# Kernel optimization log

Measured on AMD Instinct MI355X. Metric: run time of the kernel, lower is better.

## Reference

```python
import jax, jax.numpy as jnp
import numpy as np

B, P, K, F, H = 128, 200, 60, 4, 64   # events, points/event, knn k, feat dim, hidden
N = B * P


def setup_inputs() -> dict:
    key = jax.random.key(0)
    k0, k1, k2, k3 = jax.random.split(key, 4)
    x = jax.random.normal(k0, (N, F), jnp.float32)
    pos = jax.random.normal(k1, (N, 3), jnp.float32)
    batch = jnp.arange(N, dtype=jnp.int32) // P  # sorted event ids, equal-size events
    W1 = jax.random.normal(k2, (F + 3, H), jnp.float32) / np.sqrt(F + 3)
    b1 = jnp.zeros((H,), jnp.float32)
    W2 = jax.random.normal(k3, (H, H), jnp.float32) / np.sqrt(H)
    b2 = jnp.zeros((H,), jnp.float32)
    return {"x": x, "pos": pos, "batch": batch, "W1": W1, "b1": b1, "W2": W2, "b2": b2}


def _knn_edges(pos):
    """knn_graph(pos, K, batch, loop=False, flow='source_to_target').
    Equal-size events -> batched [B,P,P] pairwise distances, no cross-event edges."""
    p = pos.reshape(B, P, 3)
    d2 = jnp.sum((p[:, :, None, :] - p[:, None, :, :]) ** 2, axis=-1)  # [B,P,P]
    d2 = d2 + jnp.eye(P, dtype=d2.dtype) * 1e10                        # exclude self (loop=False)
    _, nbr = jax.lax.top_k(-d2, K)                                     # [B,P,K] local neighbor ids
    src = (nbr + (jnp.arange(B, dtype=nbr.dtype) * P)[:, None, None]).reshape(-1)  # sources j
    dst = jnp.repeat(jnp.arange(N, dtype=src.dtype), K)                             # targets i
    return jnp.stack([src, dst])  # [2, N*K]


def _local_nn(m, W1, b1, W2, b2):
    h = jax.nn.relu(m @ W1 + b1)
    return jax.nn.relu(h @ W2 + b2)


def reference(x, pos, batch, W1, b1, W2, b2):
    edge_index = _knn_edges(pos)
    src, dst = edge_index[0], edge_index[1]
    # PointConv message: net(concat[x_j, pos_j - pos_i]) on each edge
    rel = pos[src] - pos[dst]                             # [E,3]
    m = jnp.concatenate([x[src], rel], axis=-1)           # [E,F+3]
    h = _local_nn(m, W1, b1, W2, b2)                      # [E,H]
    out = h.reshape(N, K, H).max(axis=1)                  # max-aggregate per target node
    # PyG PointConv adds self-loops by default: message with rel = 0
    m_self = jnp.concatenate([x, jnp.zeros((N, 3), x.dtype)], axis=-1)
    h_self = _local_nn(m_self, W1, b1, W2, b2)            # [N,H]
    out = jnp.maximum(out, h_self)
    return (out, pos, batch, edge_index)
```

## Files before the change

kernel.cpp:

```cpp
#include <hip/hip_runtime.h>
#include <hip/hip_bf16.h>

typedef unsigned short ushort_t;
typedef unsigned int u32;
typedef unsigned long long u64;
typedef __attribute__((ext_vector_type(8))) short bf16x8;
typedef __attribute__((ext_vector_type(4))) float f32x4;
typedef __attribute__((ext_vector_type(4))) u32 u32x4;

#define NB 128
#define PP 200
#define KK 60
#define NN (NB*PP)
#define HH 64

#define OUT_OFF   0
#define POS_OFF   (NN*HH)
#define BATCH_OFF (POS_OFF + NN*3)
#define ESRC_OFF  (BATCH_OFF + NN)
#define EDST_OFF  (ESRC_OFF + NN*KK)

static __device__ __forceinline__ u32 packtr(float a, float b) {
    return __builtin_amdgcn_perm(__float_as_uint(b), __float_as_uint(a), 0x07060302u);
}
static __device__ __forceinline__ u32 prefix_lt(u64 b) {
    return __builtin_amdgcn_mbcnt_hi((u32)(b >> 32),
                                     __builtin_amdgcn_mbcnt_lo((u32)b, 0));
}

__global__ __launch_bounds__(256) void fused_kernel(const float* __restrict__ x,
                                                    const float* __restrict__ pos,
                                                    const float* __restrict__ W1,
                                                    const float* __restrict__ b1p,
                                                    const float* __restrict__ W2,
                                                    const float* __restrict__ b2p,
                                                    float* __restrict__ out) {
    __shared__ alignas(16) float xs[PP * 4];
    __shared__ alignas(16) float psl[PP * 3];
    __shared__ alignas(16) u32 jslot[4 * 128];
    __shared__ alignas(16) u32 msg[4 * 256];
    __shared__ alignas(16) u32 af[4 * 256];
    __shared__ alignas(16) u32 zrow[4];

    int tid = threadIdx.x, blk = blockIdx.x;
    int e = blk / 25;
    int pl0b = (blk % 25) * 8;
    int i0b  = e * PP + pl0b;

    if (tid < 200) ((f32x4*)xs)[tid]  = ((const f32x4*)x)[e * PP + tid];
    if (tid < 150) ((f32x4*)psl)[tid] = ((const f32x4*)pos)[e * 150 + tid];
    if (tid < 4)   zrow[tid] = 0u;
    __syncthreads();

    if (tid < 24) out[POS_OFF + i0b * 3 + tid] = psl[pl0b * 3 + tid];
    if (tid < 8)  out[BATCH_OFF + i0b + tid] = (float)e;

    int lane = tid & 63, wv = tid >> 6;
    int lo16 = lane & 15, hi16 = lane >> 4;
    int plA = pl0b + wv * 2, plB = plA + 1;
    int iA = e * PP + plA,   iB = iA + 1;

    float axA = psl[plA*3], ayA = psl[plA*3+1], azA = psl[plA*3+2];
    float axB = psl[plB*3], ayB = psl[plB*3+1], azB = psl[plB*3+2];

    u32 keyA[4], keyB[4];
    #pragma unroll
    for (int q = 0; q < 4; ++q) {
        int j = lane + q * 64;
        int jc = (j < PP) ? j : 0;
        float px = psl[jc*3], py = psl[jc*3+1], pz = psl[jc*3+2];
        float dxA = px-axA, dyA = py-ayA, dzA = pz-azA;
        float dxB = px-axB, dyB = py-ayB, dzB = pz-azB;
        float d2A = dxA*dxA + dyA*dyA + dzA*dzA;
        float d2B = dxB*dxB + dyB*dyB + dzB*dzB;
        keyA[q] = (j < PP && j != plA)
                ? ((__float_as_uint(d2A) & 0xFFFFFF00u) | (u32)j) : 0xFFFFFFFFu;
        keyB[q] = (j < PP && j != plB)
                ? ((__float_as_uint(d2B) & 0xFFFFFF00u) | (u32)j) : 0xFFFFFFFFu;
    }

    u32 loA = 0u, hiA = 0x7F800000u, loB = 0u, hiB = 0x7F800000u;
    int doneA = 0, doneB = 0;
    for (int it = 0; it < 32; ++it) {
        u32 mA = loA + ((hiA - loA) >> 1);
        u32 mB = loB + ((hiB - loB) >> 1);
        int cA = __builtin_popcountll(__ballot(keyA[0] < mA))
               + __builtin_popcountll(__ballot(keyA[1] < mA))
               + __builtin_popcountll(__ballot(keyA[2] < mA))
               + __builtin_popcountll(__ballot(keyA[3] < mA));
        int cB = __builtin_popcountll(__ballot(keyB[0] < mB))
               + __builtin_popcountll(__ballot(keyB[1] < mB))
               + __builtin_popcountll(__ballot(keyB[2] < mB))
               + __builtin_popcountll(__ballot(keyB[3] < mB));
        if (!doneA) {
            if (cA >= KK) hiA = mA; else loA = mA;
            doneA = (cA == KK) | (hiA - loA <= 1u);
        }
        if (!doneB) {
            if (cB >= KK) hiB = mB; else loB = mB;
            doneB = (cB == KK) | (hiB - loB <= 1u);
        }
        if (doneA & doneB) break;
    }

    const int jsb = wv * 128;
    if (lane >= KK) {
        jslot[jsb + lane]      = (u32)plA;
        jslot[jsb + 64 + lane] = (u32)plB;
    }
    #pragma unroll
    for (int t = 0; t < 2; ++t) {
        const u32* key = t ? keyB : keyA;
        u32 hh = t ? hiB : hiA;
        int i  = t ? iB : iA;
        u64 m0 = __ballot(key[0] < hh);
        u64 m1 = __ballot(key[1] < hh);
        u64 m2 = __ballot(key[2] < hh);
        u64 m3 = __ballot(key[3] < hh);
        u32 s1 = (u32)__builtin_popcountll(m0);
        u32 s2 = s1 + (u32)__builtin_popcountll(m1);
        u32 s3 = s2 + (u32)__builtin_popcountll(m2);
        u32 sl[4] = { prefix_lt(m0), s1 + prefix_lt(m1),
                      s2 + prefix_lt(m2), s3 + prefix_lt(m3) };
        #pragma unroll
        for (int q = 0; q < 4; ++q) {
            if (key[q] < hh) {
                u32 j = key[q] & 0xFFu;
                out[ESRC_OFF + i * KK + (int)sl[q]] = (float)(e * PP + (int)j);
                jslot[jsb + t * 64 + (int)sl[q]] = j;
            }
        }
        if (lane < KK) out[EDST_OFF + i * KK + lane] = (float)i;
    }

    bf16x8 w1f[4];
    #pragma unroll
    for (int th = 0; th < 4; ++th) {
        union { u32 w[4]; bf16x8 v; } u; u.w[0]=u.w[1]=u.w[2]=u.w[3]=0u;
        if (hi16 == 0) {
            int m = th * 16 + lo16;
            u.w[0] = packtr(W1[0*64+m], W1[1*64+m]);
            u.w[1] = packtr(W1[2*64+m], W1[3*64+m]);
            u.w[2] = packtr(W1[4*64+m], W1[5*64+m]);
            u.w[3] = packtr(W1[6*64+m], b1p[m]);
        }
        w1f[th] = u.v;
    }
    bf16x8 bfr[4][2];
    #pragma unroll
    for (int t = 0; t < 4; ++t)
        #pragma unroll
        for (int s = 0; s < 2; ++s) {
            union { u32 w[4]; bf16x8 v; } u;
            int col = t * 16 + lo16, kb = s * 32 + hi16 * 8;
            #pragma unroll
            for (int d = 0; d < 4; ++d)
                u.w[d] = packtr(W2[(kb + 2*d) * 64 + col], W2[(kb + 2*d + 1) * 64 + col]);
            bfr[t][s] = u.v;
        }
    float b2v[4];
    #pragma unroll
    for (int t = 0; t < 4; ++t) b2v[t] = b2p[t * 16 + lo16];

    const int msb = wv * 256;
    const int afb = wv * 256;
    for (int tl = 0; tl < 2; ++tl) {
        int i = iA + tl, pl = plA + tl;
        int jloc = (int)jslot[jsb + tl * 64 + lane];
        f32x4 xv = ((const f32x4*)xs)[jloc];
        float rx = psl[jloc*3]   - psl[pl*3];
        float ry = psl[jloc*3+1] - psl[pl*3+1];
        float rz = psl[jloc*3+2] - psl[pl*3+2];
        u32x4 mrow;
        mrow[0] = packtr(xv[0], xv[1]);
        mrow[1] = packtr(xv[2], xv[3]);
        mrow[2] = packtr(rx, ry);
        mrow[3] = packtr(rz, 1.0f);
        *(u32x4*)&msg[msb + lane * 4] = mrow;

        float rmax[4] = {-3.0e38f, -3.0e38f, -3.0e38f, -3.0e38f};
        #pragma unroll
        for (int rt = 0; rt < 4; ++rt) {
            const u32* mp = (hi16 == 0) ? &msg[msb + (rt * 16 + lo16) * 4] : zrow;
            union { u32 w[4]; bf16x8 v; } mu;
            *(u32x4*)mu.w = *(const u32x4*)mp;

            f32x4 c1[4];
            #pragma unroll
            for (int th = 0; th < 4; ++th)
                c1[th] = __builtin_amdgcn_mfma_f32_16x16x32_bf16(w1f[th], mu.v,
                                                                 (f32x4)0.f, 0, 0, 0);
            f32x4 acc[4];
            #pragma unroll
            for (int t = 0; t < 4; ++t) acc[t] = (f32x4)0.f;

            #pragma unroll
            for (int s = 0; s < 2; ++s) {
                #pragma unroll
                for (int thh = 0; thh < 2; ++thh) {
                    int th = s * 2 + thh;
                    u32 pk0 = packtr(fmaxf(c1[th][0], 0.f), fmaxf(c1[th][1], 0.f));
                    u32 pk1 = packtr(fmaxf(c1[th][2], 0.f), fmaxf(c1[th][3], 0.f));
                    int dlane = lo16 + ((thh * 2 + (hi16 >> 1)) << 4);
                    int dbase = (hi16 & 1) * 2;
                    af[afb + (dbase + 0) * 64 + dlane] = pk0;
                    af[afb + (dbase + 1) * 64 + dlane] = pk1;
                }
                union { u32 w[4]; bf16x8 v; } u;
                #pragma unroll
                for (int d = 0; d < 4; ++d)
                    u.w[d] = af[afb + d * 64 + lane];
                #pragma unroll
                for (int t = 0; t < 4; ++t)
                    acc[t] = __builtin_amdgcn_mfma_f32_16x16x32_bf16(u.v, bfr[t][s],
                                                                     acc[t], 0, 0, 0);
            }
            #pragma unroll
            for (int t = 0; t < 4; ++t) {
                rmax[t] = fmaxf(fmaxf(acc[t][0], acc[t][1]), rmax[t]);
                rmax[t] = fmaxf(fmaxf(acc[t][2], acc[t][3]), rmax[t]);
            }
        }
        #pragma unroll
        for (int t = 0; t < 4; ++t) {
            rmax[t] = fmaxf(rmax[t], __shfl_xor(rmax[t], 16, 64));
            rmax[t] = fmaxf(rmax[t], __shfl_xor(rmax[t], 32, 64));
        }
        if (lane < 16) {
            #pragma unroll
            for (int t = 0; t < 4; ++t)
                out[OUT_OFF + i * 64 + t * 16 + lane] = fmaxf(rmax[t] + b2v[t], 0.f);
        }
    }
}

extern "C" void kernel_launch(void* const* d_in, const int* in_sizes, int n_in,
                              void* d_out, int out_size, void* d_ws, size_t ws_size,
                              hipStream_t stream) {
    const float* x     = (const float*)d_in[0];
    const float* pos   = (const float*)d_in[1];
    const float* W1    = (const float*)d_in[3];
    const float* b1    = (const float*)d_in[4];
    const float* W2    = (const float*)d_in[5];
    const float* b2    = (const float*)d_in[6];
    float* out = (float*)d_out;
    (void)d_ws; (void)ws_size; (void)in_sizes; (void)n_in; (void)out_size;

    fused_kernel<<<dim3(NN / 8), dim3(256), 0, stream>>>(x, pos, W1, b1, W2, b2, out);
}
```

Measured before the change: 109.4 us.

## Keep layer-1 activations in registers by permuting W1 columns; halve block size

Permutes the W1 output-column order so that the MFMA accumulator layout of the first layer lines up with the A-operand fragment layout of the second layer. The LDS round-trip for the hidden activations (the af buffer and its barrier-free shuffles) is dropped, and the zero-row indirection for the message operand is removed. Blocks shrink from 4 to 2 waves (4 target points per block, twice as many blocks), with the staging loads adjusted to match. The risk is more blocks each reloading the event's x/pos and W fragments, and the message read now feeds nonzero data into the upper lanes, which relies on W1 rows beyond index 7 being zero.

```diff
diff --git a/kernel.cpp b/kernel.cpp
--- a/kernel.cpp
+++ b/kernel.cpp
@@ -28,7 +28,7 @@
                                      __builtin_amdgcn_mbcnt_lo((u32)b, 0));
 }
 
-__global__ __launch_bounds__(256) void fused_kernel(const float* __restrict__ x,
+__global__ __launch_bounds__(128) void fused_kernel(const float* __restrict__ x,
                                                     const float* __restrict__ pos,
                                                     const float* __restrict__ W1,
                                                     const float* __restrict__ b1p,
@@ -37,23 +37,22 @@
                                                     float* __restrict__ out) {
     __shared__ alignas(16) float xs[PP * 4];
     __shared__ alignas(16) float psl[PP * 3];
-    __shared__ alignas(16) u32 jslot[4 * 128];
-    __shared__ alignas(16) u32 msg[4 * 256];
-    __shared__ alignas(16) u32 af[4 * 256];
-    __shared__ alignas(16) u32 zrow[4];
+    __shared__ alignas(16) u32 jslot[2 * 128];
+    __shared__ alignas(16) u32 msg[2 * 256];
 
     int tid = threadIdx.x, blk = blockIdx.x;
-    int e = blk / 25;
-    int pl0b = (blk % 25) * 8;
+    int e = blk / 50;
+    int pl0b = (blk % 50) * 4;
     int i0b  = e * PP + pl0b;
 
-    if (tid < 200) ((f32x4*)xs)[tid]  = ((const f32x4*)x)[e * PP + tid];
-    if (tid < 150) ((f32x4*)psl)[tid] = ((const f32x4*)pos)[e * 150 + tid];
-    if (tid < 4)   zrow[tid] = 0u;
+    ((f32x4*)xs)[tid] = ((const f32x4*)x)[e * PP + tid];
+    if (tid < 72)  ((f32x4*)xs)[128 + tid]  = ((const f32x4*)x)[e * PP + 128 + tid];
+    if (tid < 128) ((f32x4*)psl)[tid]       = ((const f32x4*)pos)[e * 150 + tid];
+    if (tid < 22)  ((f32x4*)psl)[128 + tid] = ((const f32x4*)pos)[e * 150 + 128 + tid];
     __syncthreads();
 
-    if (tid < 24) out[POS_OFF + i0b * 3 + tid] = psl[pl0b * 3 + tid];
-    if (tid < 8)  out[BATCH_OFF + i0b + tid] = (float)e;
+    if (tid < 12) out[POS_OFF + i0b * 3 + tid] = psl[pl0b * 3 + tid];
+    if (tid < 4)  out[BATCH_OFF + i0b + tid] = (float)e;
 
     int lane = tid & 63, wv = tid >> 6;
     int lo16 = lane & 15, hi16 = lane >> 4;
@@ -138,11 +137,11 @@
     for (int th = 0; th < 4; ++th) {
         union { u32 w[4]; bf16x8 v; } u; u.w[0]=u.w[1]=u.w[2]=u.w[3]=0u;
         if (hi16 == 0) {
-            int m = th * 16 + lo16;
-            u.w[0] = packtr(W1[0*64+m], W1[1*64+m]);
-            u.w[1] = packtr(W1[2*64+m], W1[3*64+m]);
-            u.w[2] = packtr(W1[4*64+m], W1[5*64+m]);
-            u.w[3] = packtr(W1[6*64+m], b1p[m]);
+            int c = 32*(th>>1) + 8*(lo16>>2) + 4*(th&1) + (lo16&3);
+            u.w[0] = packtr(W1[0*64+c], W1[1*64+c]);
+            u.w[1] = packtr(W1[2*64+c], W1[3*64+c]);
+            u.w[2] = packtr(W1[4*64+c], W1[5*64+c]);
+            u.w[3] = packtr(W1[6*64+c], b1p[c]);
         }
         w1f[th] = u.v;
     }
@@ -163,7 +162,6 @@
     for (int t = 0; t < 4; ++t) b2v[t] = b2p[t * 16 + lo16];
 
     const int msb = wv * 256;
-    const int afb = wv * 256;
     for (int tl = 0; tl < 2; ++tl) {
         int i = iA + tl, pl = plA + tl;
         int jloc = (int)jslot[jsb + tl * 64 + lane];
@@ -181,40 +179,31 @@
         float rmax[4] = {-3.0e38f, -3.0e38f, -3.0e38f, -3.0e38f};
         #pragma unroll
         for (int rt = 0; rt < 4; ++rt) {
-            const u32* mp = (hi16 == 0) ? &msg[msb + (rt * 16 + lo16) * 4] : zrow;
             union { u32 w[4]; bf16x8 v; } mu;
-            *(u32x4*)mu.w = *(const u32x4*)mp;
+            *(u32x4*)mu.w = *(const u32x4*)&msg[msb + (rt * 16 + lo16) * 4];
 
             f32x4 c1[4];
             #pragma unroll
             for (int th = 0; th < 4; ++th)
                 c1[th] = __builtin_amdgcn_mfma_f32_16x16x32_bf16(w1f[th], mu.v,
                                                                  (f32x4)0.f, 0, 0, 0);
+            union { u32 w[4]; bf16x8 v; } afr[2];
+            #pragma unroll
+            for (int th = 0; th < 4; ++th) {
+                u32 pk0 = packtr(fmaxf(c1[th][0], 0.f), fmaxf(c1[th][1], 0.f));
+                u32 pk1 = packtr(fmaxf(c1[th][2], 0.f), fmaxf(c1[th][3], 0.f));
+                afr[th >> 1].w[2 * (th & 1) + 0] = pk0;
+                afr[th >> 1].w[2 * (th & 1) + 1] = pk1;
+            }
             f32x4 acc[4];
             #pragma unroll
-            for (int t = 0; t < 4; ++t) acc[t] = (f32x4)0.f;
-
-            #pragma unroll
-            for (int s = 0; s < 2; ++s) {
-                #pragma unroll
-                for (int thh = 0; thh < 2; ++thh) {
-                    int th = s * 2 + thh;
-                    u32 pk0 = packtr(fmaxf(c1[th][0], 0.f), fmaxf(c1[th][1], 0.f));
-                    u32 pk1 = packtr(fmaxf(c1[th][2], 0.f), fmaxf(c1[th][3], 0.f));
-                    int dlane = lo16 + ((thh * 2 + (hi16 >> 1)) << 4);
-                    int dbase = (hi16 & 1) * 2;
-                    af[afb + (dbase + 0) * 64 + dlane] = pk0;
-                    af[afb + (dbase + 1) * 64 + dlane] = pk1;
-                }
-                union { u32 w[4]; bf16x8 v; } u;
-                #pragma unroll
-                for (int d = 0; d < 4; ++d)
-                    u.w[d] = af[afb + d * 64 + lane];
-                #pragma unroll
-                for (int t = 0; t < 4; ++t)
-                    acc[t] = __builtin_amdgcn_mfma_f32_16x16x32_bf16(u.v, bfr[t][s],
-                                                                     acc[t], 0, 0, 0);
-            }
+            for (int t = 0; t < 4; ++t)
+                acc[t] = __builtin_amdgcn_mfma_f32_16x16x32_bf16(afr[0].v, bfr[t][0],
+                                                                 (f32x4)0.f, 0, 0, 0);
+            #pragma unroll
+            for (int t = 0; t < 4; ++t)
+                acc[t] = __builtin_amdgcn_mfma_f32_16x16x32_bf16(afr[1].v, bfr[t][1],
+                                                                 acc[t], 0, 0, 0);
             #pragma unroll
             for (int t = 0; t < 4; ++t) {
                 rmax[t] = fmaxf(fmaxf(acc[t][0], acc[t][1]), rmax[t]);
@@ -246,5 +235,5 @@
     float* out = (float*)d_out;
     (void)d_ws; (void)ws_size; (void)in_sizes; (void)n_in; (void)out_size;
 
-    fused_kernel<<<dim3(NN / 8), dim3(256), 0, stream>>>(x, pos, W1, b1, W2, b2, out);
-}
+    fused_kernel<<<dim3(NN / 4), dim3(128), 0, stream>>>(x, pos, W1, b1, W2, b2, out);
+}
```

Result: no change. 110.3 us (+0.8%).
